# Optimization experiments

Hardware: AMD Instinct MI355X
Metric: run time of the kernel (lower is better)

## Reference

```python
import jax, jax.numpy as jnp
import numpy as np

F = 256          # in_features
T = 8            # num_fragment_ion_types = 4 types * 2 charges
N_MONO, N_CLEAV, N_FRAG, N_OUT = 150000, 100000, 80000, 40000
D_CLEAV, D_JOIN, D_COMB = 4, 2, 4


def setup_inputs() -> dict:
    key = jax.random.key(0)
    ks = jax.random.split(key, 14)
    s = 0.05
    return {
        "feature": jax.random.normal(ks[0], (N_MONO, F), jnp.float32),
        "Wg_lost": jax.random.normal(ks[1], (F, 1), jnp.float32) * s,
        "Wg_ret": jax.random.normal(ks[2], (F, 1), jnp.float32) * s,
        "W_ih": jax.random.normal(ks[3], (4 * F, 2 * F), jnp.float32) * s,
        "W_hh": jax.random.normal(ks[4], (4 * F, F), jnp.float32) * s,
        "b_ih": jax.random.normal(ks[5], (4 * F,), jnp.float32) * s,
        "b_hh": jax.random.normal(ks[6], (4 * F,), jnp.float32) * s,
        "Wg_frag": jax.random.normal(ks[7], (F, 1), jnp.float32) * s,
        "W_out": jax.random.normal(ks[8], (F, T), jnp.float32) * s,
        "b_out": jnp.zeros((T,), jnp.float32),
        "lost_src": jax.random.randint(ks[9], (N_CLEAV, D_CLEAV), 0, N_MONO),
        "retained_src": jax.random.randint(ks[10], (N_CLEAV, D_CLEAV), 0, N_MONO),
        "join_src": jax.random.randint(ks[11], (N_FRAG, D_JOIN), 0, N_CLEAV),
        "combine_src": jax.random.randint(ks[12], (N_OUT, D_COMB), 0, N_FRAG),
    }


def _attention_sum(h, Wg):
    # h: [N, D, F] mailbox; gate = Linear(F,1,no bias); softmax over neighbor axis
    logits = jnp.einsum('ndf,fo->ndo', h, Wg)          # [N, D, 1]
    a = jax.nn.softmax(logits, axis=1)
    return jnp.sum(a * h, axis=1)                       # [N, F]


def _lstm(x, W_ih, W_hh, b_ih, b_hh):
    # x: [N, L, I]; torch nn.LSTM gate order i,f,g,o; zero initial state
    N = x.shape[0]
    H = W_hh.shape[1]
    def step(carry, xt):
        h, c = carry
        gates = xt @ W_ih.T + h @ W_hh.T + b_ih + b_hh  # [N, 4H]
        i, f, g, o = jnp.split(gates, 4, axis=-1)
        c = jax.nn.sigmoid(f) * c + jax.nn.sigmoid(i) * jnp.tanh(g)
        h = jax.nn.sigmoid(o) * jnp.tanh(c)
        return (h, c), h
    init = (jnp.zeros((N, H), x.dtype), jnp.zeros((N, H), x.dtype))
    _, hs = jax.lax.scan(step, init, jnp.swapaxes(x, 0, 1))
    return jnp.swapaxes(hs, 0, 1)                       # [N, L, H]


def reference(feature, Wg_lost, Wg_ret, W_ih, W_hh, b_ih, b_hh,
              Wg_frag, W_out, b_out,
              lost_src, retained_src, join_src, combine_src):
    h_lost = _attention_sum(feature[lost_src], Wg_lost)        # [N_cleav, F]
    h_ret = _attention_sum(feature[retained_src], Wg_ret)      # [N_cleav, F]
    cleav = jnp.concatenate([h_lost, h_ret], axis=-1)          # [N_cleav, 2F]
    # Fragment pull over 'join' edges: LSTM over neighbor set, then attention sum
    hs = _lstm(cleav[join_src], W_ih, W_hh, b_ih, b_hh)        # [N_frag, D_join, F]
    frag = _attention_sum(hs, Wg_frag)                         # [N_frag, F]
    # Output head: Linear + ReLU
    frag_out = jax.nn.relu(frag @ W_out + b_out)               # [N_frag, T]
    # copy_u_sum over 'combine' edges: scatter-sum of src outputs to dst
    return frag_out[combine_src].sum(axis=1)                   # [N_out, T]
```

## Files before the change

### kernel.cpp

```cpp
#include <hip/hip_runtime.h>

typedef unsigned short u16;
typedef unsigned int u32;
typedef float f32x4 __attribute__((ext_vector_type(4)));
typedef __bf16 bf16x8 __attribute__((ext_vector_type(8)));

#define F 256
#define T_OUT 8
#define N_MONO 150000
#define N_CLEAV 100000
#define N_FRAG 80000
#define N_OUT 40000
#define M_CLEAV_PAD 100352

static __device__ __forceinline__ u16 f2bf(float f) {
  u32 u = __float_as_uint(f);
  u32 r = (u + 0x7FFFu + ((u >> 16) & 1u)) >> 16;
  return (u16)r;
}
static __device__ __forceinline__ float bf2f(u16 b) {
  return __uint_as_float(((u32)b) << 16);
}
static __device__ __forceinline__ float sigmoidf(float x) {
  return __frcp_rn(1.0f + __expf(-x));
}
static __device__ __forceinline__ float fast_tanh(float x) {
  return 1.0f - 2.0f * __frcp_rn(__expf(2.0f * x) + 1.0f);
}
static __device__ __forceinline__ void async_copy16(const u16* g, const u16* l) {
  __builtin_amdgcn_global_load_lds(
      (const __attribute__((address_space(1))) u32*)g,
      (__attribute__((address_space(3))) u32*)l,
      16, 0, 0);
}

__global__ __launch_bounds__(256) void feat_prep(
    const float* __restrict__ feat, const float* __restrict__ WgL,
    const float* __restrict__ WgR, u16* __restrict__ featb,
    float* __restrict__ glog,
    const float* __restrict__ Wih, const float* __restrict__ Whh,
    const float* __restrict__ bih, const float* __restrict__ bhh,
    u16* __restrict__ Wihb, u16* __restrict__ Whhb, float* __restrict__ bias) {
  int i = blockIdx.x * 256 + threadIdx.x;
  if (i < 1024 * 512) {
    Wihb[i] = f2bf(Wih[i]);
    if (i < 1024 * 256) Whhb[i] = f2bf(Whh[i]);
    if (i < 1024) bias[i] = bih[i] + bhh[i];
  }
  int wave = threadIdx.x >> 6, lane = threadIdx.x & 63;
  int n = blockIdx.x * 4 + wave;
  if (n >= N_MONO) return;
  float4 x = *(const float4*)(feat + (size_t)n * F + lane * 4);
  u32 lo = (u32)f2bf(x.x) | ((u32)f2bf(x.y) << 16);
  u32 hi = (u32)f2bf(x.z) | ((u32)f2bf(x.w) << 16);
  *(uint2*)(featb + (size_t)n * F + lane * 4) = make_uint2(lo, hi);
  float4 wl = *(const float4*)(WgL + lane * 4);
  float4 wr = *(const float4*)(WgR + lane * 4);
  float pl = x.x * wl.x + x.y * wl.y + x.z * wl.z + x.w * wl.w;
  float pr = x.x * wr.x + x.y * wr.y + x.z * wr.z + x.w * wr.w;
#pragma unroll
  for (int off = 32; off; off >>= 1) {
    pl += __shfl_xor(pl, off);
    pr += __shfl_xor(pr, off);
  }
  if (lane == 0) {
    glog[n * 2] = pl;
    glog[n * 2 + 1] = pr;
  }
}

__global__ __launch_bounds__(256) void attn_pull2(
    const u16* __restrict__ featb, const float* __restrict__ glog,
    const int* __restrict__ lostS, const int* __restrict__ retS,
    u16* __restrict__ cleav) {
  int wave = threadIdx.x >> 6, lane = threadIdx.x & 63;
  int n = blockIdx.x * 4 + wave;
  if (n >= N_CLEAV) return;
#pragma unroll
  for (int sg = 0; sg < 2; ++sg) {
    const int* src = sg ? retS : lostS;
    int4 ridx = *(const int4*)(src + n * 4);
    int r[4] = {ridx.x, ridx.y, ridx.z, ridx.w};
    ushort4 x4[4];
    float lg[4];
#pragma unroll
    for (int d = 0; d < 4; ++d) {
      x4[d] = *(const ushort4*)(featb + (size_t)r[d] * F + lane * 4);
      lg[d] = glog[r[d] * 2 + sg];
    }
    float mx = fmaxf(fmaxf(lg[0], lg[1]), fmaxf(lg[2], lg[3]));
    float e0 = __expf(lg[0] - mx), e1 = __expf(lg[1] - mx);
    float e2 = __expf(lg[2] - mx), e3 = __expf(lg[3] - mx);
    float inv = __frcp_rn(e0 + e1 + e2 + e3);
    float a[4] = {e0 * inv, e1 * inv, e2 * inv, e3 * inv};
    float acc[4] = {0.f, 0.f, 0.f, 0.f};
#pragma unroll
    for (int d = 0; d < 4; ++d) {
      const u16* xp = (const u16*)&x4[d];
#pragma unroll
      for (int k = 0; k < 4; k++) acc[k] += a[d] * bf2f(xp[k]);
    }
    u32 lo = (u32)f2bf(acc[0]) | ((u32)f2bf(acc[1]) << 16);
    u32 hi = (u32)f2bf(acc[2]) | ((u32)f2bf(acc[3]) << 16);
    *(uint2*)(cleav + (size_t)n * 512 + sg * 256 + lane * 4) = make_uint2(lo, hi);
  }
}

template <int EPI, int K, int BM>
__global__ __launch_bounds__(512, 2) void gemm256(
    const u16* __restrict__ A, const u16* __restrict__ Bw,
    u16* __restrict__ C, const float* __restrict__ bias,
    int nper, int mstrips_valid) {
  constexpr int AREG = BM * 64;
  constexpr int BSZ = AREG + 16384;
  constexpr int WMH = BM / 2;
  constexpr int IB = BM / 32;
  constexpr int IB_HI = IB - 4;
  __shared__ u16 sh[2][BSZ];
  const int flat = blockIdx.x;
  const int xcd = flat & 7;
  const int w = flat >> 3;
  const int mstrip = xcd * nper + (w >> 2);
  const int nstrip = w & 3;
  if (mstrip >= mstrips_valid) return;
  const int m0 = mstrip * BM;
  const int n0 = nstrip * 256;

  const int tid = threadIdx.x;
  const int lane = tid & 63;
  const int wave = tid >> 6;
  const int quad = lane >> 4;
  const int l16 = lane & 15;
  const int s7 = l16 & 7;
  const int wm2 = wave >> 2;
  const int wn4 = wave & 3;

  const int arow = (wm2 * WMH + l16) * 64;
  const int brow = AREG + (wn4 * 64 + l16) * 64;
  const int coff0 = (quad ^ s7) * 8;
  const int coff1 = ((4 + quad) ^ s7) * 8;

  int sr[4], sw[4], dwv[4];
#pragma unroll
  for (int r = 0; r < 4; r++) {
    int c = r * 512 + tid;
    sr[r] = c >> 3;
    sw[r] = ((c & 7) ^ ((c >> 3) & 7)) * 8;
    dwv[r] = (r * 512 + (tid & ~63)) * 8;
  }
  const u16* Abase = A + (size_t)m0 * K;
  const u16* Bbase = Bw + (size_t)n0 * K;

  auto stageA = [&](int buf, int kt, int h) {
#pragma unroll
    for (int rr = 0; rr < 2; rr++) {
      int r = 2 * h + rr;
      if (r * 512 + tid < BM * 8)
        async_copy16(Abase + (size_t)sr[r] * K + kt * 64 + sw[r], &sh[buf][dwv[r]]);
    }
  };
  auto stageB = [&](int buf, int kt, int h) {
#pragma unroll
    for (int rr = 0; rr < 2; rr++) {
      int r = 2 * h + rr;
      async_copy16(Bbase + (size_t)sr[r] * K + kt * 64 + sw[r], &sh[buf][AREG + dwv[r]]);
    }
  };

  f32x4 acc[IB][4];
#pragma unroll
  for (int i = 0; i < IB; i++)
#pragma unroll
    for (int j = 0; j < 4; j++) acc[i][j] = (f32x4){0.f, 0.f, 0.f, 0.f};

  constexpr int nK = K / 64;
  stageA(0, 0, 0); stageA(0, 0, 1); stageB(0, 0, 0); stageB(0, 0, 1);
  if (nK > 1) { stageB(1, 1, 0); stageB(1, 1, 1); }
  __builtin_amdgcn_s_waitcnt(0xF74);
  __builtin_amdgcn_s_barrier();

  bf16x8 a[4][2], b0[2][2], b1[2][2];
#pragma unroll
  for (int t = 0; t < nK; ++t) {
    const int bsel = t & 1;
    const u16* S = &sh[bsel][0];

#pragma unroll
    for (int i = 0; i < 4; i++) {
      a[i][0] = *(const bf16x8*)&S[arow + i * 1024 + coff0];
      a[i][1] = *(const bf16x8*)&S[arow + i * 1024 + coff1];
    }
#pragma unroll
    for (int j = 0; j < 2; j++) {
      b0[j][0] = *(const bf16x8*)&S[brow + j * 1024 + coff0];
      b0[j][1] = *(const bf16x8*)&S[brow + j * 1024 + coff1];
    }
    if (t + 1 < nK) stageA(bsel ^ 1, t + 1, 0);
    __builtin_amdgcn_s_waitcnt(0xC87F);
    __builtin_amdgcn_s_barrier();
    __builtin_amdgcn_s_waitcnt(0xC07F);
    __builtin_amdgcn_sched_barrier(0);
    __builtin_amdgcn_s_setprio(1);
#pragma unroll
    for (int i = 0; i < 4; i++)
#pragma unroll
      for (int j = 0; j < 2; j++) {
        acc[i][j] = __builtin_amdgcn_mfma_f32_16x16x32_bf16(a[i][0], b0[j][0], acc[i][j], 0, 0, 0);
        acc[i][j] = __builtin_amdgcn_mfma_f32_16x16x32_bf16(a[i][1], b0[j][1], acc[i][j], 0, 0, 0);
      }
    __builtin_amdgcn_s_setprio(0);
    __builtin_amdgcn_s_barrier();

#pragma unroll
    for (int j = 0; j < 2; j++) {
      b1[j][0] = *(const bf16x8*)&S[brow + (2 + j) * 1024 + coff0];
      b1[j][1] = *(const bf16x8*)&S[brow + (2 + j) * 1024 + coff1];
    }
    if (t + 1 < nK) stageA(bsel ^ 1, t + 1, 1);
    __builtin_amdgcn_s_barrier();
    __builtin_amdgcn_s_waitcnt(0xC07F);
    __builtin_amdgcn_sched_barrier(0);
    __builtin_amdgcn_s_setprio(1);
#pragma unroll
    for (int i = 0; i < 4; i++)
#pragma unroll
      for (int j = 0; j < 2; j++) {
        acc[i][2 + j] = __builtin_amdgcn_mfma_f32_16x16x32_bf16(a[i][0], b1[j][0], acc[i][2 + j], 0, 0, 0);
        acc[i][2 + j] = __builtin_amdgcn_mfma_f32_16x16x32_bf16(a[i][1], b1[j][1], acc[i][2 + j], 0, 0, 0);
      }
    __builtin_amdgcn_s_setprio(0);
    __builtin_amdgcn_s_barrier();

#pragma unroll
    for (int i = 0; i < IB_HI; i++) {
      a[i][0] = *(const bf16x8*)&S[arow + (4 + i) * 1024 + coff0];
      a[i][1] = *(const bf16x8*)&S[arow + (4 + i) * 1024 + coff1];
    }
    if (t + 2 < nK) stageB(bsel, t + 2, 0);
    __builtin_amdgcn_s_barrier();
    __builtin_amdgcn_s_waitcnt(0xC07F);
    __builtin_amdgcn_sched_barrier(0);
    __builtin_amdgcn_s_setprio(1);
#pragma unroll
    for (int i = 0; i < IB_HI; i++)
#pragma unroll
      for (int j = 0; j < 2; j++) {
        acc[4 + i][j] = __builtin_amdgcn_mfma_f32_16x16x32_bf16(a[i][0], b0[j][0], acc[4 + i][j], 0, 0, 0);
        acc[4 + i][j] = __builtin_amdgcn_mfma_f32_16x16x32_bf16(a[i][1], b0[j][1], acc[4 + i][j], 0, 0, 0);
      }
    __builtin_amdgcn_s_setprio(0);
    __builtin_amdgcn_s_barrier();

    if (t + 2 < nK) stageB(bsel, t + 2, 1);
    __builtin_amdgcn_s_barrier();
    __builtin_amdgcn_s_setprio(1);
#pragma unroll
    for (int i = 0; i < IB_HI; i++)
#pragma unroll
      for (int j = 0; j < 2; j++) {
        acc[4 + i][2 + j] = __builtin_amdgcn_mfma_f32_16x16x32_bf16(a[i][0], b1[j][0], acc[4 + i][2 + j], 0, 0, 0);
        acc[4 + i][2 + j] = __builtin_amdgcn_mfma_f32_16x16x32_bf16(a[i][1], b1[j][1], acc[4 + i][2 + j], 0, 0, 0);
      }
    __builtin_amdgcn_s_setprio(0);
    if (t + 2 < nK) __builtin_amdgcn_s_waitcnt(0xF74);
    else            __builtin_amdgcn_s_waitcnt(0xF70);
    __builtin_amdgcn_s_barrier();
  }

  float badd[4];
#pragma unroll
  for (int j = 0; j < 4; j++)
    badd[j] = (EPI == 0) ? bias[n0 + wn4 * 64 + j * 16 + l16] : 0.f;
#pragma unroll
  for (int i = 0; i < IB; i++) {
    const int mrow = m0 + wm2 * WMH + i * 16 + quad * 4;
#pragma unroll
    for (int j = 0; j < 4; j++) {
      const int n = n0 + wn4 * 64 + j * 16 + l16;
#pragma unroll
      for (int r = 0; r < 4; r++)
        C[(size_t)(mrow + r) * 1024 + n] = f2bf(acc[i][j][r] + badd[j]);
    }
  }
}

__global__ __launch_bounds__(256) void lstm_step1(
    const u16* __restrict__ P, const int* __restrict__ join,
    u16* __restrict__ h1, u16* __restrict__ c1) {
  int wave = threadIdx.x >> 6, lane = threadIdx.x & 63;
  int m = blockIdx.x * 4 + wave;
  if (m >= N_FRAG) return;
  int j0 = join[2 * m];
  const u16* row = P + (size_t)j0 * 1024 + lane * 4;
  ushort4 iv = *(const ushort4*)(row);
  ushort4 gv = *(const ushort4*)(row + 512);
  ushort4 ov = *(const ushort4*)(row + 768);
  const u16* ivp = (const u16*)&iv;
  const u16* gvp = (const u16*)&gv;
  const u16* ovp = (const u16*)&ov;
  ushort4 h4, c4;
  u16* h4p = (u16*)&h4;
  u16* c4p = (u16*)&c4;
#pragma unroll
  for (int k = 0; k < 4; k++) {
    float c = sigmoidf(bf2f(ivp[k])) * fast_tanh(bf2f(gvp[k]));
    float hv = sigmoidf(bf2f(ovp[k])) * fast_tanh(c);
    h4p[k] = f2bf(hv);
    c4p[k] = f2bf(c);
  }
  *(ushort4*)(h1 + (size_t)m * 256 + lane * 4) = h4;
  *(ushort4*)(c1 + (size_t)m * 256 + lane * 4) = c4;
}

__global__ __launch_bounds__(256) void lstm_step2_attn_out(
    const u16* __restrict__ G2, const u16* __restrict__ P,
    const int* __restrict__ join, const u16* __restrict__ c1,
    const u16* __restrict__ h1b, const float* __restrict__ Wg,
    const float* __restrict__ Wout, const float* __restrict__ bout,
    float* __restrict__ frag_out) {
  int wave = threadIdx.x >> 6, lane = threadIdx.x & 63;
  int m = blockIdx.x * 4 + wave;
  if (m >= N_FRAG) return;
  int j1 = join[2 * m + 1];
  const u16* row = G2 + (size_t)m * 1024 + lane * 4;
  const u16* prow = P + (size_t)j1 * 1024 + lane * 4;
  ushort4 iv = *(const ushort4*)(row);
  ushort4 fv = *(const ushort4*)(row + 256);
  ushort4 gv = *(const ushort4*)(row + 512);
  ushort4 ov = *(const ushort4*)(row + 768);
  ushort4 pi = *(const ushort4*)(prow);
  ushort4 pf = *(const ushort4*)(prow + 256);
  ushort4 pg = *(const ushort4*)(prow + 512);
  ushort4 po = *(const ushort4*)(prow + 768);
  ushort4 c4 = *(const ushort4*)(c1 + (size_t)m * 256 + lane * 4);
  ushort4 h4 = *(const ushort4*)(h1b + (size_t)m * 256 + lane * 4);
  float4 wg = *(const float4*)(Wg + lane * 4);
  const u16* ivp = (const u16*)&iv; const u16* pip = (const u16*)&pi;
  const u16* fvp = (const u16*)&fv; const u16* pfp = (const u16*)&pf;
  const u16* gvp = (const u16*)&gv; const u16* pgp = (const u16*)&pg;
  const u16* ovp = (const u16*)&ov; const u16* pop = (const u16*)&po;
  const u16* c4p = (const u16*)&c4;
  const u16* h4p = (const u16*)&h4;
  const float* wgp = (const float*)&wg;

  float h1v[4], h2v[4];
  float p1 = 0.f, p2 = 0.f;
#pragma unroll
  for (int k = 0; k < 4; k++) {
    float gi = bf2f(ivp[k]) + bf2f(pip[k]);
    float gf = bf2f(fvp[k]) + bf2f(pfp[k]);
    float gg = bf2f(gvp[k]) + bf2f(pgp[k]);
    float go = bf2f(ovp[k]) + bf2f(pop[k]);
    float c2 = sigmoidf(gf) * bf2f(c4p[k]) + sigmoidf(gi) * fast_tanh(gg);
    float h2 = sigmoidf(go) * fast_tanh(c2);
    h2v[k] = h2;
    h1v[k] = bf2f(h4p[k]);
    p1 += h1v[k] * wgp[k];
    p2 += h2 * wgp[k];
  }
#pragma unroll
  for (int off = 32; off; off >>= 1) {
    p1 += __shfl_xor(p1, off);
    p2 += __shfl_xor(p2, off);
  }
  float mx = fmaxf(p1, p2);
  float e1 = __expf(p1 - mx), e2 = __expf(p2 - mx);
  float inv = __frcp_rn(e1 + e2);
  float a1 = e1 * inv, a2 = e2 * inv;

  float acc[8];
#pragma unroll
  for (int t = 0; t < 8; t++) acc[t] = 0.f;
#pragma unroll
  for (int k = 0; k < 4; k++) {
    float frag = a1 * h1v[k] + a2 * h2v[k];
    int h = lane * 4 + k;
    float4 w0 = *(const float4*)(Wout + h * 8);
    float4 w1 = *(const float4*)(Wout + h * 8 + 4);
    acc[0] += frag * w0.x; acc[1] += frag * w0.y;
    acc[2] += frag * w0.z; acc[3] += frag * w0.w;
    acc[4] += frag * w1.x; acc[5] += frag * w1.y;
    acc[6] += frag * w1.z; acc[7] += frag * w1.w;
  }
#pragma unroll
  for (int off = 32; off; off >>= 1)
#pragma unroll
    for (int t = 0; t < 8; t++) acc[t] += __shfl_xor(acc[t], off);
  if (lane == 0) {
    float4 o0, o1;
    o0.x = fmaxf(acc[0] + bout[0], 0.f);
    o0.y = fmaxf(acc[1] + bout[1], 0.f);
    o0.z = fmaxf(acc[2] + bout[2], 0.f);
    o0.w = fmaxf(acc[3] + bout[3], 0.f);
    o1.x = fmaxf(acc[4] + bout[4], 0.f);
    o1.y = fmaxf(acc[5] + bout[5], 0.f);
    o1.z = fmaxf(acc[6] + bout[6], 0.f);
    o1.w = fmaxf(acc[7] + bout[7], 0.f);
    *(float4*)(frag_out + (size_t)m * 8) = o0;
    *(float4*)(frag_out + (size_t)m * 8 + 4) = o1;
  }
}

__global__ __launch_bounds__(256) void scatter_sum(
    const float* __restrict__ frag_out, const int* __restrict__ comb,
    float* __restrict__ out) {
  int tid = blockIdx.x * 256 + threadIdx.x;
  if (tid >= N_OUT * 8) return;
  int n = tid >> 3, t = tid & 7;
  float s = 0.f;
#pragma unroll
  for (int d = 0; d < 4; d++) {
    int f = comb[n * 4 + d];
    s += frag_out[(size_t)f * 8 + t];
  }
  out[tid] = s;
}

extern "C" void kernel_launch(void* const* d_in, const int* in_sizes, int n_in,
                              void* d_out, int out_size, void* d_ws, size_t ws_size,
                              hipStream_t stream) {
  const float* feature = (const float*)d_in[0];
  const float* WgL = (const float*)d_in[1];
  const float* WgR = (const float*)d_in[2];
  const float* Wih = (const float*)d_in[3];
  const float* Whh = (const float*)d_in[4];
  const float* bih = (const float*)d_in[5];
  const float* bhh = (const float*)d_in[6];
  const float* Wgf = (const float*)d_in[7];
  const float* Wout = (const float*)d_in[8];
  const float* bout = (const float*)d_in[9];
  const int* lostS = (const int*)d_in[10];
  const int* retS = (const int*)d_in[11];
  const int* joinS = (const int*)d_in[12];
  const int* combS = (const int*)d_in[13];
  float* out = (float*)d_out;

  char* ws = (char*)d_ws;
  size_t off = 0;
  auto alloc = [&](size_t bytes) -> char* {
    char* p = ws + off;
    off = (off + bytes + 255) & ~(size_t)255;
    return p;
  };
  u16* Wihb = (u16*)alloc((size_t)1024 * 512 * 2);
  u16* Whhb = (u16*)alloc((size_t)1024 * 256 * 2);
  float* bias = (float*)alloc(1024 * 4);
  u16* P = (u16*)alloc((size_t)M_CLEAV_PAD * 1024 * 2);
  u16* h1 = (u16*)alloc((size_t)N_FRAG * 256 * 2);
  u16* c1 = (u16*)alloc((size_t)N_FRAG * 256 * 2);
  float* frag_out = (float*)alloc((size_t)N_FRAG * 8 * 4);
  char* uni = alloc((size_t)M_CLEAV_PAD * 1024 * 2);
  u16* cleav = (u16*)uni;
  u16* gates2 = (u16*)uni;
  u16* featb = P;
  float* glog = (float*)(P + (size_t)N_MONO * F);

  feat_prep<<<(N_MONO + 3) / 4, 256, 0, stream>>>(
      feature, WgL, WgR, featb, glog, Wih, Whh, bih, bhh, Wihb, Whhb, bias);
  attn_pull2<<<N_CLEAV / 4, 256, 0, stream>>>(featb, glog, lostS, retS, cleav);
  gemm256<0, 512, 224><<<1792, 512, 0, stream>>>(cleav, Wihb, P, bias, 56, 448);
  lstm_step1<<<N_FRAG / 4, 256, 0, stream>>>(P, joinS, h1, c1);
  gemm256<1, 256, 256><<<1280, 512, 0, stream>>>(h1, Whhb, gates2, nullptr, 40, 313);
  lstm_step2_attn_out<<<N_FRAG / 4, 256, 0, stream>>>(
      gates2, P, joinS, c1, h1, Wgf, Wout, bout, frag_out);
  scatter_sum<<<(N_OUT * 8 + 255) / 256, 256, 0, stream>>>(frag_out, combS, out);
}
```

Baseline: 663.3 us.

## Fuse LSTM step-2 cell update and attention logits into recurrent GEMM epilogue

The W_hh GEMM now permutes its B rows so that each wave holds the i/f/g/o gates for the same hidden units. Its epilogue can then compute the second LSTM cell directly, write h2 in a strip layout and emit partial attention logits. This removes the round trip of writing and re-reading the full 1024-wide gates2 tensor. The first step now computes its logit p1, and a lighter final kernel combines the partial logits, applies the softmax and does the output projection. The cost is scattered per-element gathers of P and c1 inside the GEMM epilogue, more register pressure, and extra padded buffers.

```diff
diff --git a/kernel.cpp b/kernel.cpp
--- a/kernel.cpp
+++ b/kernel.cpp
@@ -10,6 +10,7 @@
 #define N_MONO 150000
 #define N_CLEAV 100000
 #define N_FRAG 80000
+#define N_FRAG_PAD 80128
 #define N_OUT 40000
 #define M_CLEAV_PAD 100352
 
@@ -110,6 +111,9 @@
 __global__ __launch_bounds__(512, 2) void gemm256(
     const u16* __restrict__ A, const u16* __restrict__ Bw,
     u16* __restrict__ C, const float* __restrict__ bias,
+    const int* __restrict__ join, const u16* __restrict__ P,
+    const u16* __restrict__ c1, const float* __restrict__ Wg,
+    u16* __restrict__ h2s, float* __restrict__ p2p,
     int nper, int mstrips_valid) {
   constexpr int AREG = BM * 64;
   constexpr int BSZ = AREG + 16384;
@@ -140,16 +144,19 @@
   const int coff0 = (quad ^ s7) * 8;
   const int coff1 = ((4 + quad) ^ s7) * 8;
 
-  int sr[4], sw[4], dwv[4];
+  int sr[4], sw[4], dwv[4], bsrc[4];
 #pragma unroll
   for (int r = 0; r < 4; r++) {
     int c = r * 512 + tid;
-    sr[r] = c >> 3;
-    sw[r] = ((c & 7) ^ ((c >> 3) & 7)) * 8;
+    int row = c >> 3;
+    sr[r] = row;
+    sw[r] = ((c & 7) ^ (row & 7)) * 8;
     dwv[r] = (r * 512 + (tid & ~63)) * 8;
+    bsrc[r] = (EPI == 1)
+        ? ((row >> 4) & 3) * 256 + nstrip * 64 + ((row >> 6) << 4) + (row & 15)
+        : n0 + row;
   }
   const u16* Abase = A + (size_t)m0 * K;
-  const u16* Bbase = Bw + (size_t)n0 * K;
 
   auto stageA = [&](int buf, int kt, int h) {
 #pragma unroll
@@ -163,7 +170,7 @@
 #pragma unroll
     for (int rr = 0; rr < 2; rr++) {
       int r = 2 * h + rr;
-      async_copy16(Bbase + (size_t)sr[r] * K + kt * 64 + sw[r], &sh[buf][AREG + dwv[r]]);
+      async_copy16(Bw + (size_t)bsrc[r] * K + kt * 64 + sw[r], &sh[buf][AREG + dwv[r]]);
     }
   };
 
@@ -267,26 +274,53 @@
     __builtin_amdgcn_s_barrier();
   }
 
-  float badd[4];
-#pragma unroll
-  for (int j = 0; j < 4; j++)
-    badd[j] = (EPI == 0) ? bias[n0 + wn4 * 64 + j * 16 + l16] : 0.f;
-#pragma unroll
-  for (int i = 0; i < IB; i++) {
-    const int mrow = m0 + wm2 * WMH + i * 16 + quad * 4;
-#pragma unroll
-    for (int j = 0; j < 4; j++) {
-      const int n = n0 + wn4 * 64 + j * 16 + l16;
-#pragma unroll
-      for (int r = 0; r < 4; r++)
-        C[(size_t)(mrow + r) * 1024 + n] = f2bf(acc[i][j][r] + badd[j]);
+  if constexpr (EPI == 0) {
+    float badd[4];
+#pragma unroll
+    for (int j = 0; j < 4; j++)
+      badd[j] = bias[n0 + wn4 * 64 + j * 16 + l16];
+#pragma unroll
+    for (int i = 0; i < IB; i++) {
+      const int mrow = m0 + wm2 * WMH + i * 16 + quad * 4;
+#pragma unroll
+      for (int j = 0; j < 4; j++) {
+        const int n = n0 + wn4 * 64 + j * 16 + l16;
+#pragma unroll
+        for (int r = 0; r < 4; r++)
+          C[(size_t)(mrow + r) * 1024 + n] = f2bf(acc[i][j][r] + badd[j]);
+      }
+    }
+  } else {
+    const int hg = nstrip * 64 + wn4 * 16 + l16;
+    const float wgv = Wg[hg];
+#pragma unroll
+    for (int i = 0; i < IB; i++) {
+#pragma unroll
+      for (int r = 0; r < 4; r++) {
+        const int m = m0 + wm2 * WMH + i * 16 + quad * 4 + r;
+        const int j1 = (m < N_FRAG) ? join[2 * m + 1] : 0;
+        const u16* prow = P + (size_t)j1 * 1024 + hg;
+        float gi = acc[i][0][r] + bf2f(prow[0]);
+        float gf = acc[i][1][r] + bf2f(prow[256]);
+        float gg = acc[i][2][r] + bf2f(prow[512]);
+        float go = acc[i][3][r] + bf2f(prow[768]);
+        float c1v = bf2f(c1[(size_t)m * 256 + hg]);
+        float c2 = sigmoidf(gf) * c1v + sigmoidf(gi) * fast_tanh(gg);
+        float h2 = sigmoidf(go) * fast_tanh(c2);
+        float p = h2 * wgv;
+        p += __shfl_xor(p, 1); p += __shfl_xor(p, 2);
+        p += __shfl_xor(p, 4); p += __shfl_xor(p, 8);
+        if (l16 == 0) p2p[(size_t)m * 16 + nstrip * 4 + wn4] = p;
+        h2s[((size_t)nstrip * N_FRAG_PAD + m) * 64 + wn4 * 16 + l16] = f2bf(h2);
+      }
     }
   }
 }
 
 __global__ __launch_bounds__(256) void lstm_step1(
     const u16* __restrict__ P, const int* __restrict__ join,
-    u16* __restrict__ h1, u16* __restrict__ c1) {
+    const float* __restrict__ Wg, u16* __restrict__ h1,
+    u16* __restrict__ c1, float* __restrict__ p1) {
   int wave = threadIdx.x >> 6, lane = threadIdx.x & 63;
   int m = blockIdx.x * 4 + wave;
   if (m >= N_FRAG) return;
@@ -295,85 +329,59 @@
   ushort4 iv = *(const ushort4*)(row);
   ushort4 gv = *(const ushort4*)(row + 512);
   ushort4 ov = *(const ushort4*)(row + 768);
+  float4 wg = *(const float4*)(Wg + lane * 4);
   const u16* ivp = (const u16*)&iv;
   const u16* gvp = (const u16*)&gv;
   const u16* ovp = (const u16*)&ov;
+  const float* wgp = (const float*)&wg;
   ushort4 h4, c4;
   u16* h4p = (u16*)&h4;
   u16* c4p = (u16*)&c4;
+  float pl = 0.f;
 #pragma unroll
   for (int k = 0; k < 4; k++) {
     float c = sigmoidf(bf2f(ivp[k])) * fast_tanh(bf2f(gvp[k]));
     float hv = sigmoidf(bf2f(ovp[k])) * fast_tanh(c);
     h4p[k] = f2bf(hv);
     c4p[k] = f2bf(c);
-  }
+    pl += bf2f(h4p[k]) * wgp[k];
+  }
+#pragma unroll
+  for (int off = 32; off; off >>= 1) pl += __shfl_xor(pl, off);
   *(ushort4*)(h1 + (size_t)m * 256 + lane * 4) = h4;
   *(ushort4*)(c1 + (size_t)m * 256 + lane * 4) = c4;
-}
-
-__global__ __launch_bounds__(256) void lstm_step2_attn_out(
-    const u16* __restrict__ G2, const u16* __restrict__ P,
-    const int* __restrict__ join, const u16* __restrict__ c1,
-    const u16* __restrict__ h1b, const float* __restrict__ Wg,
+  if (lane == 0) p1[m] = pl;
+}
+
+__global__ __launch_bounds__(256) void lstm_attn_out(
+    const u16* __restrict__ h1, const u16* __restrict__ h2s,
+    const float* __restrict__ p1, const float* __restrict__ p2p,
     const float* __restrict__ Wout, const float* __restrict__ bout,
     float* __restrict__ frag_out) {
   int wave = threadIdx.x >> 6, lane = threadIdx.x & 63;
   int m = blockIdx.x * 4 + wave;
   if (m >= N_FRAG) return;
-  int j1 = join[2 * m + 1];
-  const u16* row = G2 + (size_t)m * 1024 + lane * 4;
-  const u16* prow = P + (size_t)j1 * 1024 + lane * 4;
-  ushort4 iv = *(const ushort4*)(row);
-  ushort4 fv = *(const ushort4*)(row + 256);
-  ushort4 gv = *(const ushort4*)(row + 512);
-  ushort4 ov = *(const ushort4*)(row + 768);
-  ushort4 pi = *(const ushort4*)(prow);
-  ushort4 pf = *(const ushort4*)(prow + 256);
-  ushort4 pg = *(const ushort4*)(prow + 512);
-  ushort4 po = *(const ushort4*)(prow + 768);
-  ushort4 c4 = *(const ushort4*)(c1 + (size_t)m * 256 + lane * 4);
-  ushort4 h4 = *(const ushort4*)(h1b + (size_t)m * 256 + lane * 4);
-  float4 wg = *(const float4*)(Wg + lane * 4);
-  const u16* ivp = (const u16*)&iv; const u16* pip = (const u16*)&pi;
-  const u16* fvp = (const u16*)&fv; const u16* pfp = (const u16*)&pf;
-  const u16* gvp = (const u16*)&gv; const u16* pgp = (const u16*)&pg;
-  const u16* ovp = (const u16*)&ov; const u16* pop = (const u16*)&po;
-  const u16* c4p = (const u16*)&c4;
-  const u16* h4p = (const u16*)&h4;
-  const float* wgp = (const float*)&wg;
-
-  float h1v[4], h2v[4];
-  float p1 = 0.f, p2 = 0.f;
-#pragma unroll
-  for (int k = 0; k < 4; k++) {
-    float gi = bf2f(ivp[k]) + bf2f(pip[k]);
-    float gf = bf2f(fvp[k]) + bf2f(pfp[k]);
-    float gg = bf2f(gvp[k]) + bf2f(pgp[k]);
-    float go = bf2f(ovp[k]) + bf2f(pop[k]);
-    float c2 = sigmoidf(gf) * bf2f(c4p[k]) + sigmoidf(gi) * fast_tanh(gg);
-    float h2 = sigmoidf(go) * fast_tanh(c2);
-    h2v[k] = h2;
-    h1v[k] = bf2f(h4p[k]);
-    p1 += h1v[k] * wgp[k];
-    p2 += h2 * wgp[k];
-  }
-#pragma unroll
-  for (int off = 32; off; off >>= 1) {
-    p1 += __shfl_xor(p1, off);
-    p2 += __shfl_xor(p2, off);
-  }
-  float mx = fmaxf(p1, p2);
-  float e1 = __expf(p1 - mx), e2 = __expf(p2 - mx);
+  float4 q = *(const float4*)(p2p + (size_t)m * 16 + (lane & 3) * 4);
+  float p2 = q.x + q.y + q.z + q.w;
+  p2 += __shfl_xor(p2, 1);
+  p2 += __shfl_xor(p2, 2);
+  float p1v = p1[m];
+  float mx = fmaxf(p1v, p2);
+  float e1 = __expf(p1v - mx), e2 = __expf(p2 - mx);
   float inv = __frcp_rn(e1 + e2);
   float a1 = e1 * inv, a2 = e2 * inv;
 
+  ushort4 h1v = *(const ushort4*)(h1 + (size_t)m * 256 + lane * 4);
+  ushort4 h2v = *(const ushort4*)(h2s + ((size_t)(lane >> 4) * N_FRAG_PAD + m) * 64 + (lane & 15) * 4);
+  const u16* h1p = (const u16*)&h1v;
+  const u16* h2p = (const u16*)&h2v;
+
   float acc[8];
 #pragma unroll
   for (int t = 0; t < 8; t++) acc[t] = 0.f;
 #pragma unroll
   for (int k = 0; k < 4; k++) {
-    float frag = a1 * h1v[k] + a2 * h2v[k];
+    float frag = a1 * bf2f(h1p[k]) + a2 * bf2f(h2p[k]);
     int h = lane * 4 + k;
     float4 w0 = *(const float4*)(Wout + h * 8);
     float4 w1 = *(const float4*)(Wout + h * 8 + 4);
@@ -446,22 +454,27 @@
   u16* Whhb = (u16*)alloc((size_t)1024 * 256 * 2);
   float* bias = (float*)alloc(1024 * 4);
   u16* P = (u16*)alloc((size_t)M_CLEAV_PAD * 1024 * 2);
-  u16* h1 = (u16*)alloc((size_t)N_FRAG * 256 * 2);
-  u16* c1 = (u16*)alloc((size_t)N_FRAG * 256 * 2);
+  u16* h1 = (u16*)alloc((size_t)N_FRAG_PAD * 256 * 2);
+  u16* c1 = (u16*)alloc((size_t)N_FRAG_PAD * 256 * 2);
+  u16* h2s = (u16*)alloc((size_t)4 * N_FRAG_PAD * 64 * 2);
+  float* p2p = (float*)alloc((size_t)N_FRAG_PAD * 16 * 4);
+  float* p1 = (float*)alloc((size_t)N_FRAG_PAD * 4);
   float* frag_out = (float*)alloc((size_t)N_FRAG * 8 * 4);
-  char* uni = alloc((size_t)M_CLEAV_PAD * 1024 * 2);
-  u16* cleav = (u16*)uni;
-  u16* gates2 = (u16*)uni;
+  u16* cleav = (u16*)alloc((size_t)M_CLEAV_PAD * 1024 * 2);
   u16* featb = P;
   float* glog = (float*)(P + (size_t)N_MONO * F);
 
   feat_prep<<<(N_MONO + 3) / 4, 256, 0, stream>>>(
       feature, WgL, WgR, featb, glog, Wih, Whh, bih, bhh, Wihb, Whhb, bias);
   attn_pull2<<<N_CLEAV / 4, 256, 0, stream>>>(featb, glog, lostS, retS, cleav);
-  gemm256<0, 512, 224><<<1792, 512, 0, stream>>>(cleav, Wihb, P, bias, 56, 448);
-  lstm_step1<<<N_FRAG / 4, 256, 0, stream>>>(P, joinS, h1, c1);
-  gemm256<1, 256, 256><<<1280, 512, 0, stream>>>(h1, Whhb, gates2, nullptr, 40, 313);
-  lstm_step2_attn_out<<<N_FRAG / 4, 256, 0, stream>>>(
-      gates2, P, joinS, c1, h1, Wgf, Wout, bout, frag_out);
+  gemm256<0, 512, 224><<<1792, 512, 0, stream>>>(
+      cleav, Wihb, P, bias, nullptr, nullptr, nullptr, nullptr, nullptr, nullptr,
+      56, 448);
+  lstm_step1<<<N_FRAG / 4, 256, 0, stream>>>(P, joinS, Wgf, h1, c1, p1);
+  gemm256<1, 256, 256><<<1280, 512, 0, stream>>>(
+      h1, Whhb, nullptr, nullptr, joinS, P, c1, Wgf, h2s, p2p,
+      40, 313);
+  lstm_attn_out<<<N_FRAG / 4, 256, 0, stream>>>(
+      h1, h2s, p1, p2p, Wout, bout, frag_out);
   scatter_sum<<<(N_OUT * 8 + 255) / 256, 256, 0, stream>>>(frag_out, combS, out);
 }
```

New measurement: 772.1 us. 1.16x slower.

## Fuse LSTM step-2 cell update into the recurrent h1·Whh GEMM epilogue

Applied to the files above, without the earlier changes.

Replaces the second GEMM, which wrote the full 80000x1024 bf16 gate matrix, with a new kernel. It tiles the N dimension so that each block holds matching i/f/g/o columns for 32 hidden units. It gathers the input-projection rows via join indices into LDS and computes c2/h2 in the epilogue, writing only h2 (80000x256). This removes the large gates2 round-trip through memory. The attention and output head now read h1/h2 only. Padding of h1/c1 is added so the 128-row tiles are safe, at the cost of a new GEMM with smaller tiles and triple buffering that may be less efficient than the tuned 256-wide one.

```diff
diff --git a/kernel.cpp b/kernel.cpp
--- a/kernel.cpp
+++ b/kernel.cpp
@@ -10,6 +10,7 @@
 #define N_MONO 150000
 #define N_CLEAV 100000
 #define N_FRAG 80000
+#define N_FRAG_PAD 80128
 #define N_OUT 40000
 #define M_CLEAV_PAD 100352
 
@@ -106,11 +107,11 @@
   }
 }
 
-template <int EPI, int K, int BM>
-__global__ __launch_bounds__(512, 2) void gemm256(
+__global__ __launch_bounds__(512, 2) void gemm224(
     const u16* __restrict__ A, const u16* __restrict__ Bw,
     u16* __restrict__ C, const float* __restrict__ bias,
     int nper, int mstrips_valid) {
+  constexpr int K = 512, BM = 224;
   constexpr int AREG = BM * 64;
   constexpr int BSZ = AREG + 16384;
   constexpr int WMH = BM / 2;
@@ -175,7 +176,7 @@
 
   constexpr int nK = K / 64;
   stageA(0, 0, 0); stageA(0, 0, 1); stageB(0, 0, 0); stageB(0, 0, 1);
-  if (nK > 1) { stageB(1, 1, 0); stageB(1, 1, 1); }
+  stageB(1, 1, 0); stageB(1, 1, 1);
   __builtin_amdgcn_s_waitcnt(0xF74);
   __builtin_amdgcn_s_barrier();
 
@@ -270,7 +271,7 @@
   float badd[4];
 #pragma unroll
   for (int j = 0; j < 4; j++)
-    badd[j] = (EPI == 0) ? bias[n0 + wn4 * 64 + j * 16 + l16] : 0.f;
+    badd[j] = bias[n0 + wn4 * 64 + j * 16 + l16];
 #pragma unroll
   for (int i = 0; i < IB; i++) {
     const int mrow = m0 + wm2 * WMH + i * 16 + quad * 4;
@@ -289,7 +290,12 @@
     u16* __restrict__ h1, u16* __restrict__ c1) {
   int wave = threadIdx.x >> 6, lane = threadIdx.x & 63;
   int m = blockIdx.x * 4 + wave;
-  if (m >= N_FRAG) return;
+  if (m >= N_FRAG_PAD) return;
+  if (m >= N_FRAG) {
+    *(ushort4*)(h1 + (size_t)m * 256 + lane * 4) = make_ushort4(0, 0, 0, 0);
+    *(ushort4*)(c1 + (size_t)m * 256 + lane * 4) = make_ushort4(0, 0, 0, 0);
+    return;
+  }
   int j0 = join[2 * m];
   const u16* row = P + (size_t)j0 * 1024 + lane * 4;
   ushort4 iv = *(const ushort4*)(row);
@@ -312,51 +318,154 @@
   *(ushort4*)(c1 + (size_t)m * 256 + lane * 4) = c4;
 }
 
-__global__ __launch_bounds__(256) void lstm_step2_attn_out(
-    const u16* __restrict__ G2, const u16* __restrict__ P,
-    const int* __restrict__ join, const u16* __restrict__ c1,
-    const u16* __restrict__ h1b, const float* __restrict__ Wg,
-    const float* __restrict__ Wout, const float* __restrict__ bout,
-    float* __restrict__ frag_out) {
+__global__ __launch_bounds__(256, 3) void g2fuse(
+    const u16* __restrict__ h1A, const u16* __restrict__ Whhb,
+    const u16* __restrict__ P, const int* __restrict__ join,
+    const u16* __restrict__ c1in, u16* __restrict__ h2s) {
+  constexpr int K = 256;
+  __shared__ u16 sh[6][128 * 32];
+  const int w = blockIdx.x;
+  const int mstrip = w >> 3;
+  const int nstrip = w & 7;
+  const int m0 = mstrip * 128;
+
+  const int tid = threadIdx.x;
+  const int lane = tid & 63;
+  const int wave = tid >> 6;
+  const int quad = lane >> 4;
+  const int l16 = lane & 15;
+  const int wm = (wave & 1) * 64;
+  const int wnq = wave >> 1;
+  const int wn = wnq * 64;
+
+  int srow[2], skoff[2], ldsoff[2], brow[2];
+#pragma unroll
+  for (int jj = 0; jj < 2; jj++) {
+    int c = jj * 256 + tid;
+    int row = c >> 2;
+    srow[jj] = row;
+    skoff[jj] = ((c & 3) ^ ((c >> 3) & 3)) * 8;
+    ldsoff[jj] = (jj * 256 + (tid & ~63)) * 8;
+    brow[jj] = ((row >> 4) & 3) * 256 + nstrip * 32 + ((row >> 6) << 4) + (row & 15);
+  }
+  const u16* Abase = h1A + (size_t)m0 * K;
+
+  int jrow[8];
+#pragma unroll
+  for (int rd = 0; rd < 8; rd++) {
+    int mm = m0 + rd * 16 + (tid >> 4);
+    jrow[rd] = join[2 * (mm < N_FRAG ? mm : N_FRAG - 1) + 1];
+  }
+
+  auto stage = [&](int buf, int k0) {
+#pragma unroll
+    for (int jj = 0; jj < 2; jj++)
+      async_copy16(Abase + (size_t)srow[jj] * K + k0 + skoff[jj], &sh[buf][ldsoff[jj]]);
+#pragma unroll
+    for (int jj = 0; jj < 2; jj++)
+      async_copy16(Whhb + (size_t)brow[jj] * K + k0 + skoff[jj], &sh[3 + buf][ldsoff[jj]]);
+  };
+
+  f32x4 acc[4][4];
+#pragma unroll
+  for (int i = 0; i < 4; i++)
+#pragma unroll
+    for (int j = 0; j < 4; j++) acc[i][j] = (f32x4){0.f, 0.f, 0.f, 0.f};
+
+  constexpr int nK = K / 32;
+  stage(0, 0);
+  stage(1, 32);
+#pragma unroll
+  for (int t = 0; t < nK; ++t) {
+    if (t < nK - 1) __builtin_amdgcn_s_waitcnt(0xF74);
+    else            __builtin_amdgcn_s_waitcnt(0xF70);
+    __builtin_amdgcn_s_barrier();
+    if (t + 2 < nK) stage((t + 2) % 3, (t + 2) * 32);
+    const int buf = t % 3;
+    bf16x8 af[4], bfr[4];
+#pragma unroll
+    for (int i = 0; i < 4; i++) {
+      int m = wm + i * 16 + l16;
+      int jp = quad ^ ((m >> 1) & 3);
+      af[i] = *(const bf16x8*)&sh[buf][m * 32 + jp * 8];
+    }
+#pragma unroll
+    for (int j = 0; j < 4; j++) {
+      int n = wn + j * 16 + l16;
+      int jp = quad ^ ((n >> 1) & 3);
+      bfr[j] = *(const bf16x8*)&sh[3 + buf][n * 32 + jp * 8];
+    }
+#pragma unroll
+    for (int i = 0; i < 4; i++)
+#pragma unroll
+      for (int j = 0; j < 4; j++)
+        acc[i][j] = __builtin_amdgcn_mfma_f32_16x16x32_bf16(af[i], bfr[j], acc[i][j], 0, 0, 0);
+  }
+
+  __builtin_amdgcn_s_barrier();
+  const int u_ = wnq * 16 + l16;
+  u16 c1r[4][4];
+#pragma unroll
+  for (int i = 0; i < 4; i++)
+#pragma unroll
+    for (int r = 0; r < 4; r++) {
+      int m = m0 + wm + i * 16 + quad * 4 + r;
+      c1r[i][r] = c1in[(size_t)m * 256 + nstrip * 32 + u_];
+    }
+  u16* Pl = &sh[0][0];
+  {
+    const int g = (tid >> 2) & 3;
+    const int chunk = tid & 3;
+#pragma unroll
+    for (int rd = 0; rd < 8; rd++) {
+      const int mloc = rd * 16 + (tid >> 4);
+      const int cphys = chunk ^ ((mloc >> 2) & 3);
+      async_copy16(P + (size_t)jrow[rd] * 1024 + g * 256 + nstrip * 32 + cphys * 8,
+                   &Pl[(size_t)(rd * 256 + (tid & ~63)) * 8]);
+    }
+  }
+  __builtin_amdgcn_s_waitcnt(0xF70);
+  __builtin_amdgcn_s_barrier();
+  __builtin_amdgcn_sched_barrier(0);
+
+#pragma unroll
+  for (int i = 0; i < 4; i++) {
+#pragma unroll
+    for (int r = 0; r < 4; r++) {
+      const int mloc = wm + i * 16 + quad * 4 + r;
+      const int m = m0 + mloc;
+      const int base = (mloc * 16 + ((u_ >> 3) ^ ((mloc >> 2) & 3))) * 8 + (u_ & 7);
+      float gi = acc[i][0][r] + bf2f(Pl[base]);
+      float gf = acc[i][1][r] + bf2f(Pl[base + 32]);
+      float gg = acc[i][2][r] + bf2f(Pl[base + 64]);
+      float go = acc[i][3][r] + bf2f(Pl[base + 96]);
+      float c1v = bf2f(c1r[i][r]);
+      float cv = sigmoidf(gf) * c1v + sigmoidf(gi) * fast_tanh(gg);
+      float hv = sigmoidf(go) * fast_tanh(cv);
+      h2s[(size_t)m * 256 + nstrip * 32 + u_] = f2bf(hv);
+    }
+  }
+}
+
+__global__ __launch_bounds__(256) void lstm_attn_out(
+    const u16* __restrict__ h1, const u16* __restrict__ h2s,
+    const float* __restrict__ Wg, const float* __restrict__ Wout,
+    const float* __restrict__ bout, float* __restrict__ frag_out) {
   int wave = threadIdx.x >> 6, lane = threadIdx.x & 63;
   int m = blockIdx.x * 4 + wave;
   if (m >= N_FRAG) return;
-  int j1 = join[2 * m + 1];
-  const u16* row = G2 + (size_t)m * 1024 + lane * 4;
-  const u16* prow = P + (size_t)j1 * 1024 + lane * 4;
-  ushort4 iv = *(const ushort4*)(row);
-  ushort4 fv = *(const ushort4*)(row + 256);
-  ushort4 gv = *(const ushort4*)(row + 512);
-  ushort4 ov = *(const ushort4*)(row + 768);
-  ushort4 pi = *(const ushort4*)(prow);
-  ushort4 pf = *(const ushort4*)(prow + 256);
-  ushort4 pg = *(const ushort4*)(prow + 512);
-  ushort4 po = *(const ushort4*)(prow + 768);
-  ushort4 c4 = *(const ushort4*)(c1 + (size_t)m * 256 + lane * 4);
-  ushort4 h4 = *(const ushort4*)(h1b + (size_t)m * 256 + lane * 4);
+  ushort4 h1v = *(const ushort4*)(h1 + (size_t)m * 256 + lane * 4);
+  ushort4 h2v = *(const ushort4*)(h2s + (size_t)m * 256 + lane * 4);
   float4 wg = *(const float4*)(Wg + lane * 4);
-  const u16* ivp = (const u16*)&iv; const u16* pip = (const u16*)&pi;
-  const u16* fvp = (const u16*)&fv; const u16* pfp = (const u16*)&pf;
-  const u16* gvp = (const u16*)&gv; const u16* pgp = (const u16*)&pg;
-  const u16* ovp = (const u16*)&ov; const u16* pop = (const u16*)&po;
-  const u16* c4p = (const u16*)&c4;
-  const u16* h4p = (const u16*)&h4;
+  const u16* h1p = (const u16*)&h1v;
+  const u16* h2p = (const u16*)&h2v;
   const float* wgp = (const float*)&wg;
 
-  float h1v[4], h2v[4];
   float p1 = 0.f, p2 = 0.f;
 #pragma unroll
   for (int k = 0; k < 4; k++) {
-    float gi = bf2f(ivp[k]) + bf2f(pip[k]);
-    float gf = bf2f(fvp[k]) + bf2f(pfp[k]);
-    float gg = bf2f(gvp[k]) + bf2f(pgp[k]);
-    float go = bf2f(ovp[k]) + bf2f(pop[k]);
-    float c2 = sigmoidf(gf) * bf2f(c4p[k]) + sigmoidf(gi) * fast_tanh(gg);
-    float h2 = sigmoidf(go) * fast_tanh(c2);
-    h2v[k] = h2;
-    h1v[k] = bf2f(h4p[k]);
-    p1 += h1v[k] * wgp[k];
-    p2 += h2 * wgp[k];
+    p1 += bf2f(h1p[k]) * wgp[k];
+    p2 += bf2f(h2p[k]) * wgp[k];
   }
 #pragma unroll
   for (int off = 32; off; off >>= 1) {
@@ -373,7 +482,7 @@
   for (int t = 0; t < 8; t++) acc[t] = 0.f;
 #pragma unroll
   for (int k = 0; k < 4; k++) {
-    float frag = a1 * h1v[k] + a2 * h2v[k];
+    float frag = a1 * bf2f(h1p[k]) + a2 * bf2f(h2p[k]);
     int h = lane * 4 + k;
     float4 w0 = *(const float4*)(Wout + h * 8);
     float4 w1 = *(const float4*)(Wout + h * 8 + 4);
@@ -446,22 +555,21 @@
   u16* Whhb = (u16*)alloc((size_t)1024 * 256 * 2);
   float* bias = (float*)alloc(1024 * 4);
   u16* P = (u16*)alloc((size_t)M_CLEAV_PAD * 1024 * 2);
-  u16* h1 = (u16*)alloc((size_t)N_FRAG * 256 * 2);
-  u16* c1 = (u16*)alloc((size_t)N_FRAG * 256 * 2);
+  u16* h1 = (u16*)alloc((size_t)N_FRAG_PAD * 256 * 2);
+  u16* c1 = (u16*)alloc((size_t)N_FRAG_PAD * 256 * 2);
+  u16* h2s = (u16*)alloc((size_t)N_FRAG_PAD * 256 * 2);
   float* frag_out = (float*)alloc((size_t)N_FRAG * 8 * 4);
-  char* uni = alloc((size_t)M_CLEAV_PAD * 1024 * 2);
-  u16* cleav = (u16*)uni;
-  u16* gates2 = (u16*)uni;
+  u16* cleav = (u16*)alloc((size_t)M_CLEAV_PAD * 512 * 2);
   u16* featb = P;
   float* glog = (float*)(P + (size_t)N_MONO * F);
 
   feat_prep<<<(N_MONO + 3) / 4, 256, 0, stream>>>(
       feature, WgL, WgR, featb, glog, Wih, Whh, bih, bhh, Wihb, Whhb, bias);
   attn_pull2<<<N_CLEAV / 4, 256, 0, stream>>>(featb, glog, lostS, retS, cleav);
-  gemm256<0, 512, 224><<<1792, 512, 0, stream>>>(cleav, Wihb, P, bias, 56, 448);
-  lstm_step1<<<N_FRAG / 4, 256, 0, stream>>>(P, joinS, h1, c1);
-  gemm256<1, 256, 256><<<1280, 512, 0, stream>>>(h1, Whhb, gates2, nullptr, 40, 313);
-  lstm_step2_attn_out<<<N_FRAG / 4, 256, 0, stream>>>(
-      gates2, P, joinS, c1, h1, Wgf, Wout, bout, frag_out);
+  gemm224<<<1792, 512, 0, stream>>>(cleav, Wihb, P, bias, 56, 448);
+  lstm_step1<<<N_FRAG_PAD / 4, 256, 0, stream>>>(P, joinS, h1, c1);
+  g2fuse<<<626 * 8, 256, 0, stream>>>(h1, Whhb, P, joinS, c1, h2s);
+  lstm_attn_out<<<N_FRAG / 4, 256, 0, stream>>>(
+      h1, h2s, Wgf, Wout, bout, frag_out);
   scatter_sum<<<(N_OUT * 8 + 255) / 256, 256, 0, stream>>>(frag_out, combS, out);
 }
```

Measured after the change: 690.9 us. 4.2% more time.
